# Kernel tuning notes

Measured on AMD Instinct MI355X. Metric: run time of the kernel, lower is better.

## Reference

```python
import jax, jax.numpy as jnp
import numpy as np

T = 100          # sequence length (number of GRU steps)
H = 50           # carry/hidden dim
Z = 10           # latent dim
OUT = Z + Z * (Z + 1) // 2  # 65: mean + tril Cholesky entries
LN_EPS = 1e-6    # flax LayerNorm default epsilon


def setup_inputs() -> dict:
    key = jax.random.key(0)
    ks = jax.random.split(key, 8)
    # Orthogonal-ish recurrent kernels via QR for well-conditioned dynamics
    def ortho(k):
        a = jax.random.normal(k, (H, H), dtype=jnp.float32)
        q, _ = jnp.linalg.qr(a)
        return q
    return {
        "carry_init": jax.random.normal(ks[0], (H,), dtype=jnp.float32),
        "W_hr": ortho(ks[1]), "b_hr": jnp.zeros((H,), jnp.float32),
        "s_r": jnp.ones((H,), jnp.float32), "o_r": jnp.zeros((H,), jnp.float32),
        "W_hz": ortho(ks[2]), "b_hz": jnp.zeros((H,), jnp.float32),
        "s_z": jnp.ones((H,), jnp.float32), "o_z": jnp.zeros((H,), jnp.float32),
        "W_hn": ortho(ks[3]), "b_hn": jnp.zeros((H,), jnp.float32),
        "s_n": jnp.ones((H,), jnp.float32), "o_n": jnp.zeros((H,), jnp.float32),
        "W_dense": jax.random.normal(ks[4], (H, OUT), jnp.float32) * (1.0 / jnp.sqrt(H)),
        "b_dense": jnp.zeros((OUT,), jnp.float32),
    }


def _layernorm(x, scale, bias):
    mu = jnp.mean(x, axis=-1, keepdims=True)
    var = jnp.mean(jnp.square(x - mu), axis=-1, keepdims=True)
    return (x - mu) * jax.lax.rsqrt(var + LN_EPS) * scale + bias


def reference(carry_init, W_hr, b_hr, s_r, o_r, W_hz, b_hz, s_z, o_z,
              W_hn, b_hn, s_n, o_n, W_dense, b_dense):
    # Input to the GRU is zeros((T,1)) -> cell ignores it entirely (no input kernel).
    def step(h, _):
        r = jax.nn.sigmoid(_layernorm(h @ W_hr + b_hr, s_r, o_r))
        z = jax.nn.sigmoid(_layernorm(h @ W_hz + b_hz, s_z, o_z))
        n = jnp.tanh(r * _layernorm(h @ W_hn + b_hn, s_n, o_n))
        new_h = (1.0 - z) * n + z * h
        return new_h, new_h

    _, hs = jax.lax.scan(step, carry_init, None, length=T)  # (T, H)
    out = hs @ W_dense + b_dense                              # (T, OUT)

    tril = jnp.tril_indices(Z)
    eye = jnp.eye(Z, dtype=out.dtype)

    def nat(x):
        mu, flat = x[:Z], x[Z:]
        L = jnp.zeros((Z, Z), dtype=x.dtype).at[tril].set(flat)
        d = jax.nn.softplus(jnp.diagonal(L))  # positive diagonal -> PD Sigma
        L = L.at[jnp.diag_indices(Z)].set(d)
        Sigma = L @ L.T
        # psd_solve: J = Sigma^{-1} via Cholesky solve
        J = jax.scipy.linalg.cho_solve((L, True), eye)
        h_nat = J @ mu
        return Sigma, mu, J, h_nat

    Sigma, mu, J, h_nat = jax.vmap(nat)(out)
    return Sigma, mu, J, h_nat
```

## Files before the change

kernel.cpp:

```cpp
#include <hip/hip_runtime.h>
#include <hip/hip_bf16.h>
#include <math.h>

#define T_STEPS 100
#define H_DIM   50
#define Z_DIM   10
#define OUT_DIM 65

__device__ __forceinline__ float bcast_lane(float v, int lane) {
    return __uint_as_float(__builtin_amdgcn_readlane(__float_as_uint(v), lane));
}

template<int CTRL>
__device__ __forceinline__ float dpp_mov(float x) {
    return __uint_as_float((unsigned)__builtin_amdgcn_update_dpp(
        0, (int)__float_as_uint(x), CTRL, 0xF, 0xF, true));
}

#define DPP_SHR1    0x111
#define DPP_SHR2    0x112
#define DPP_SHR4    0x114
#define DPP_SHR8    0x118
#define DPP_BCAST15 0x142
#define DPP_BCAST31 0x143

__device__ __forceinline__ void wave_sum2(float& a, float& b) {
    a += dpp_mov<DPP_SHR1>(a);    b += dpp_mov<DPP_SHR1>(b);
    a += dpp_mov<DPP_SHR2>(a);    b += dpp_mov<DPP_SHR2>(b);
    a += dpp_mov<DPP_SHR4>(a);    b += dpp_mov<DPP_SHR4>(b);
    a += dpp_mov<DPP_SHR8>(a);    b += dpp_mov<DPP_SHR8>(b);
    a += dpp_mov<DPP_BCAST15>(a); b += dpp_mov<DPP_BCAST15>(b);
    a += dpp_mov<DPP_BCAST31>(a); b += dpp_mov<DPP_BCAST31>(b);
    a = bcast_lane(a, 63);
    b = bcast_lane(b, 63);
}

__device__ __forceinline__ float fast_rcp(float x) { return __builtin_amdgcn_rcpf(x); }
__device__ __forceinline__ float fast_rsq(float x) { return __builtin_amdgcn_rsqf(x); }
__device__ __forceinline__ float fast_sigmoid(float x) {
    return fast_rcp(1.0f + __expf(-x));
}
__device__ __forceinline__ float fast_tanh(float y) {
    return 1.0f - 2.0f * fast_rcp(__expf(2.0f * y) + 1.0f);
}

__global__ __launch_bounds__(256, 1)
void gru_nat_kernel(
    const float* __restrict__ carry_init,
    const float* __restrict__ W_hr, const float* __restrict__ b_hr,
    const float* __restrict__ s_r,  const float* __restrict__ o_r,
    const float* __restrict__ W_hz, const float* __restrict__ b_hz,
    const float* __restrict__ s_z,  const float* __restrict__ o_z,
    const float* __restrict__ W_hn, const float* __restrict__ b_hn,
    const float* __restrict__ s_n,  const float* __restrict__ o_n,
    const float* __restrict__ W_dense, const float* __restrict__ b_dense,
    float* __restrict__ out)
{
    __shared__ float hs[T_STEPS][H_DIM];
    __shared__ float dense[T_STEPS][OUT_DIM];
    __shared__ float share[2][3][64];

    const int tid  = threadIdx.x;
    const int wave = tid >> 6;
    const int lane = tid & 63;

    if (wave < 3) {
        const bool valid = (lane < H_DIM);
        const int  jc    = valid ? lane : 0;

        const float* __restrict__ Wg = (wave == 0) ? W_hr : (wave == 1) ? W_hz : W_hn;
        const float* __restrict__ bg = (wave == 0) ? b_hr : (wave == 1) ? b_hz : b_hn;
        const float* __restrict__ sg = (wave == 0) ? s_r  : (wave == 1) ? s_z  : s_n;
        const float* __restrict__ og = (wave == 0) ? o_r  : (wave == 1) ? o_z  : o_n;

        float w[H_DIM];
        #pragma unroll
        for (int i = 0; i < H_DIM; ++i) w[i] = Wg[i * H_DIM + jc];
        const float bj = bg[jc], sj = sg[jc], oj = og[jc];

        float h = valid ? carry_init[jc] : 0.0f;
        const float invH = 1.0f / (float)H_DIM;

        #pragma unroll 1
        for (int t = 0; t < T_STEPS; ++t) {
            float a0 = bj, a1 = 0.0f, a2 = 0.0f, a3 = 0.0f;
            #pragma unroll
            for (int i = 0; i < 48; i += 4) {
                a0 = fmaf(bcast_lane(h, i + 0), w[i + 0], a0);
                a1 = fmaf(bcast_lane(h, i + 1), w[i + 1], a1);
                a2 = fmaf(bcast_lane(h, i + 2), w[i + 2], a2);
                a3 = fmaf(bcast_lane(h, i + 3), w[i + 3], a3);
            }
            a0 = fmaf(bcast_lane(h, 48), w[48], a0);
            a1 = fmaf(bcast_lane(h, 49), w[49], a1);
            const float a = (a0 + a2) + (a1 + a3);

            float m = valid ? a     : 0.0f;
            float q = valid ? a * a : 0.0f;
            wave_sum2(m, q);

            const float mu   = m * invH;
            const float var  = fmaxf(q * invH - mu * mu, 0.0f);
            const float gval = (a - mu) * fast_rsq(var + 1e-6f) * sj + oj;

            const float sv = (wave == 2) ? gval : fast_sigmoid(gval);
            share[t & 1][wave][lane] = sv;
            __syncthreads();

            const float r  = share[t & 1][0][lane];
            const float z  = share[t & 1][1][lane];
            const float gn = share[t & 1][2][lane];
            const float n  = fast_tanh(r * gn);
            h = n + z * (h - n);
            if (wave == 0 && valid) hs[t][lane] = h;
        }
    } else {
        #pragma unroll 1
        for (int t = 0; t < T_STEPS; ++t) __syncthreads();
    }
    __syncthreads();

    for (int idx = tid; idx < T_STEPS * OUT_DIM; idx += 256) {
        const int t = idx / OUT_DIM;
        const int o = idx - t * OUT_DIM;
        float acc = b_dense[o];
        #pragma unroll 10
        for (int i = 0; i < H_DIM; ++i)
            acc = fmaf(hs[t][i], W_dense[i * OUT_DIM + o], acc);
        dense[t][o] = acc;
    }
    __syncthreads();

    if (tid < T_STEPS) {
        const int t = tid;

        float mu[Z_DIM];
        #pragma unroll
        for (int i = 0; i < Z_DIM; ++i) mu[i] = dense[t][i];

        float L[55];
        #pragma unroll
        for (int f = 0; f < 55; ++f) L[f] = dense[t][Z_DIM + f];

        #pragma unroll
        for (int i = 0; i < Z_DIM; ++i) {
            const int   d = i * (i + 1) / 2 + i;
            const float x = L[d];
            L[d] = (x > 20.0f) ? x : log1pf(__expf(x));
        }

        float* outSigma = out;
        float* outMu    = out + 10000;
        float* outJ     = out + 11000;
        float* outHnat  = out + 21000;

        #pragma unroll
        for (int a = 0; a < Z_DIM; ++a) {
            #pragma unroll
            for (int b = 0; b <= a; ++b) {
                float s = 0.0f;
                #pragma unroll
                for (int k = 0; k <= b; ++k)
                    s = fmaf(L[a * (a + 1) / 2 + k], L[b * (b + 1) / 2 + k], s);
                outSigma[t * 100 + a * 10 + b] = s;
                outSigma[t * 100 + b * 10 + a] = s;
            }
        }

        #pragma unroll
        for (int i = 0; i < Z_DIM; ++i) outMu[t * 10 + i] = mu[i];

        #pragma unroll
        for (int i = 0; i < Z_DIM; ++i) {
            const float d = 1.0f / L[i * (i + 1) / 2 + i];
            float tmp[Z_DIM];
            #pragma unroll
            for (int k = 0; k < Z_DIM - 1; ++k) tmp[k] = 0.0f;
            #pragma unroll
            for (int k = 0; k < i; ++k) {
                float s = 0.0f;
                #pragma unroll
                for (int m = k; m < i; ++m)
                    s = fmaf(L[i * (i + 1) / 2 + m], L[m * (m + 1) / 2 + k], s);
                tmp[k] = -s * d;
            }
            #pragma unroll
            for (int k = 0; k < i; ++k) L[i * (i + 1) / 2 + k] = tmp[k];
            L[i * (i + 1) / 2 + i] = d;
        }

        float hn[Z_DIM];
        #pragma unroll
        for (int a = 0; a < Z_DIM; ++a) hn[a] = 0.0f;

        #pragma unroll
        for (int a = 0; a < Z_DIM; ++a) {
            #pragma unroll
            for (int b = 0; b <= a; ++b) {
                float s = 0.0f;
                #pragma unroll
                for (int m = a; m < Z_DIM; ++m)
                    s = fmaf(L[m * (m + 1) / 2 + a], L[m * (m + 1) / 2 + b], s);
                outJ[t * 100 + a * 10 + b] = s;
                outJ[t * 100 + b * 10 + a] = s;
                hn[a] = fmaf(s, mu[b], hn[a]);
                if (b < a) hn[b] = fmaf(s, mu[a], hn[b]);
            }
        }
        #pragma unroll
        for (int a = 0; a < Z_DIM; ++a) outHnat[t * 10 + a] = hn[a];
    }
}

extern "C" void kernel_launch(void* const* d_in, const int* in_sizes, int n_in,
                              void* d_out, int out_size, void* d_ws, size_t ws_size,
                              hipStream_t stream) {
    const float* p[15];
    for (int i = 0; i < 15; ++i) p[i] = (const float*)d_in[i];
    gru_nat_kernel<<<dim3(1), dim3(256), 0, stream>>>(
        p[0],
        p[1], p[2], p[3], p[4],
        p[5], p[6], p[7], p[8],
        p[9], p[10], p[11], p[12],
        p[13], p[14],
        (float*)d_out);
}
```

Measured before the change: 146.1 us.

## Run all GRU gates in one wave with packed fp16 dot2 matvec

The three-wave GRU recurrence becomes a single 64-lane wave that computes the r, z and n gates together. This removes the per-step block-wide barrier and the shared-memory exchange of gate values. The recurrent weights and the hidden state are packed into fp16 pairs and combined with dot2 instructions, which halves the inner-loop instruction count and the number of readlane broadcasts. The cost is three times the matvec work on one wave, plus reduced precision in the recurrence that could accumulate over 100 steps.

```diff
diff --git a/kernel.cpp b/kernel.cpp
--- a/kernel.cpp
+++ b/kernel.cpp
@@ -6,33 +6,44 @@
 #define H_DIM   50
 #define Z_DIM   10
 #define OUT_DIM 65
+#define KP      25
+
+typedef _Float16 half2v __attribute__((ext_vector_type(2)));
 
 __device__ __forceinline__ float bcast_lane(float v, int lane) {
     return __uint_as_float(__builtin_amdgcn_readlane(__float_as_uint(v), lane));
 }
-
+__device__ __forceinline__ unsigned readlane_u(unsigned v, int lane) {
+    return (unsigned)__builtin_amdgcn_readlane((int)v, lane);
+}
 template<int CTRL>
 __device__ __forceinline__ float dpp_mov(float x) {
     return __uint_as_float((unsigned)__builtin_amdgcn_update_dpp(
         0, (int)__float_as_uint(x), CTRL, 0xF, 0xF, true));
 }
-
-#define DPP_SHR1    0x111
-#define DPP_SHR2    0x112
-#define DPP_SHR4    0x114
-#define DPP_SHR8    0x118
-#define DPP_BCAST15 0x142
-#define DPP_BCAST31 0x143
-
-__device__ __forceinline__ void wave_sum2(float& a, float& b) {
-    a += dpp_mov<DPP_SHR1>(a);    b += dpp_mov<DPP_SHR1>(b);
-    a += dpp_mov<DPP_SHR2>(a);    b += dpp_mov<DPP_SHR2>(b);
-    a += dpp_mov<DPP_SHR4>(a);    b += dpp_mov<DPP_SHR4>(b);
-    a += dpp_mov<DPP_SHR8>(a);    b += dpp_mov<DPP_SHR8>(b);
-    a += dpp_mov<DPP_BCAST15>(a); b += dpp_mov<DPP_BCAST15>(b);
-    a += dpp_mov<DPP_BCAST31>(a); b += dpp_mov<DPP_BCAST31>(b);
-    a = bcast_lane(a, 63);
-    b = bcast_lane(b, 63);
+#define DPP_ROW_SHL1 0x101
+#define DPP_SHR1     0x111
+#define DPP_SHR2     0x112
+#define DPP_SHR4     0x114
+#define DPP_SHR8     0x118
+#define DPP_BCAST15  0x142
+#define DPP_BCAST31  0x143
+
+__device__ __forceinline__ unsigned pack_h2(float lo, float hi) {
+    half2v p;
+    p.x = (_Float16)lo;
+    p.y = (_Float16)hi;
+    return __builtin_bit_cast(unsigned, p);
+}
+__device__ __forceinline__ float fdot2h(unsigned a, unsigned b, float c) {
+#if __has_builtin(__builtin_amdgcn_fdot2)
+    return __builtin_amdgcn_fdot2(__builtin_bit_cast(half2v, a),
+                                  __builtin_bit_cast(half2v, b), c, false);
+#else
+    const half2v x = __builtin_bit_cast(half2v, a);
+    const half2v y = __builtin_bit_cast(half2v, b);
+    return fmaf((float)x.x, (float)y.x, fmaf((float)x.y, (float)y.y, c));
+#endif
 }
 
 __device__ __forceinline__ float fast_rcp(float x) { return __builtin_amdgcn_rcpf(x); }
@@ -58,65 +69,97 @@
 {
     __shared__ float hs[T_STEPS][H_DIM];
     __shared__ float dense[T_STEPS][OUT_DIM];
-    __shared__ float share[2][3][64];
 
     const int tid  = threadIdx.x;
-    const int wave = tid >> 6;
-    const int lane = tid & 63;
-
-    if (wave < 3) {
-        const bool valid = (lane < H_DIM);
-        const int  jc    = valid ? lane : 0;
-
-        const float* __restrict__ Wg = (wave == 0) ? W_hr : (wave == 1) ? W_hz : W_hn;
-        const float* __restrict__ bg = (wave == 0) ? b_hr : (wave == 1) ? b_hz : b_hn;
-        const float* __restrict__ sg = (wave == 0) ? s_r  : (wave == 1) ? s_z  : s_n;
-        const float* __restrict__ og = (wave == 0) ? o_r  : (wave == 1) ? o_z  : o_n;
-
-        float w[H_DIM];
-        #pragma unroll
-        for (int i = 0; i < H_DIM; ++i) w[i] = Wg[i * H_DIM + jc];
-        const float bj = bg[jc], sj = sg[jc], oj = og[jc];
+
+    if (tid < 64) {
+        const int  j     = tid;
+        const bool valid = (j < H_DIM);
+        const int  jc    = valid ? j : 0;
+
+        unsigned wr[KP], wz[KP], wn[KP];
+        #pragma unroll
+        for (int k = 0; k < KP; ++k) {
+            const float r0 = valid ? W_hr[(2 * k)     * H_DIM + jc] : 0.0f;
+            const float r1 = valid ? W_hr[(2 * k + 1) * H_DIM + jc] : 0.0f;
+            const float z0 = valid ? W_hz[(2 * k)     * H_DIM + jc] : 0.0f;
+            const float z1 = valid ? W_hz[(2 * k + 1) * H_DIM + jc] : 0.0f;
+            const float n0 = valid ? W_hn[(2 * k)     * H_DIM + jc] : 0.0f;
+            const float n1 = valid ? W_hn[(2 * k + 1) * H_DIM + jc] : 0.0f;
+            wr[k] = pack_h2(r0, r1);
+            wz[k] = pack_h2(z0, z1);
+            wn[k] = pack_h2(n0, n1);
+        }
+        const float bjr = valid ? b_hr[jc] : 0.0f;
+        const float bjz = valid ? b_hz[jc] : 0.0f;
+        const float bjn = valid ? b_hn[jc] : 0.0f;
+        const float sr  = s_r[jc], og_r = o_r[jc];
+        const float sz  = s_z[jc], og_z = o_z[jc];
+        const float sn  = s_n[jc], og_n = o_n[jc];
 
         float h = valid ? carry_init[jc] : 0.0f;
         const float invH = 1.0f / (float)H_DIM;
 
+        float    hsl = dpp_mov<DPP_ROW_SHL1>(h);
+        unsigned hpk = pack_h2(h, hsl);
+
         #pragma unroll 1
         for (int t = 0; t < T_STEPS; ++t) {
-            float a0 = bj, a1 = 0.0f, a2 = 0.0f, a3 = 0.0f;
-            #pragma unroll
-            for (int i = 0; i < 48; i += 4) {
-                a0 = fmaf(bcast_lane(h, i + 0), w[i + 0], a0);
-                a1 = fmaf(bcast_lane(h, i + 1), w[i + 1], a1);
-                a2 = fmaf(bcast_lane(h, i + 2), w[i + 2], a2);
-                a3 = fmaf(bcast_lane(h, i + 3), w[i + 3], a3);
-            }
-            a0 = fmaf(bcast_lane(h, 48), w[48], a0);
-            a1 = fmaf(bcast_lane(h, 49), w[49], a1);
-            const float a = (a0 + a2) + (a1 + a3);
-
-            float m = valid ? a     : 0.0f;
-            float q = valid ? a * a : 0.0f;
-            wave_sum2(m, q);
-
-            const float mu   = m * invH;
-            const float var  = fmaxf(q * invH - mu * mu, 0.0f);
-            const float gval = (a - mu) * fast_rsq(var + 1e-6f) * sj + oj;
-
-            const float sv = (wave == 2) ? gval : fast_sigmoid(gval);
-            share[t & 1][wave][lane] = sv;
-            __syncthreads();
-
-            const float r  = share[t & 1][0][lane];
-            const float z  = share[t & 1][1][lane];
-            const float gn = share[t & 1][2][lane];
-            const float n  = fast_tanh(r * gn);
+            float ar0 = bjr, ar1 = 0.0f;
+            float az0 = bjz, az1 = 0.0f;
+            float an0 = bjn, an1 = 0.0f;
+            #pragma unroll
+            for (int k = 0; k < KP; k += 2) {
+                const unsigned s0 = readlane_u(hpk, 2 * k);
+                ar0 = fdot2h(s0, wr[k], ar0);
+                az0 = fdot2h(s0, wz[k], az0);
+                an0 = fdot2h(s0, wn[k], an0);
+                if (k + 1 < KP) {
+                    const unsigned s1 = readlane_u(hpk, 2 * (k + 1));
+                    ar1 = fdot2h(s1, wr[k + 1], ar1);
+                    az1 = fdot2h(s1, wz[k + 1], az1);
+                    an1 = fdot2h(s1, wn[k + 1], an1);
+                }
+            }
+            const float ar = ar0 + ar1;
+            const float az = az0 + az1;
+            const float an = an0 + an1;
+
+            float mr = ar, qr = ar * ar;
+            float mz = az, qz = az * az;
+            float mn = an, qn = an * an;
+            #define STAGE(C)                                      \
+                mr += dpp_mov<C>(mr); qr += dpp_mov<C>(qr);       \
+                mz += dpp_mov<C>(mz); qz += dpp_mov<C>(qz);       \
+                mn += dpp_mov<C>(mn); qn += dpp_mov<C>(qn);
+            STAGE(DPP_SHR1) STAGE(DPP_SHR2) STAGE(DPP_SHR4)
+            STAGE(DPP_SHR8) STAGE(DPP_BCAST15) STAGE(DPP_BCAST31)
+            #undef STAGE
+            mr = bcast_lane(mr, 63); qr = bcast_lane(qr, 63);
+            mz = bcast_lane(mz, 63); qz = bcast_lane(qz, 63);
+            mn = bcast_lane(mn, 63); qn = bcast_lane(qn, 63);
+
+            const float mu_r  = mr * invH;
+            const float var_r = fmaxf(qr * invH - mu_r * mu_r, 0.0f);
+            const float g_r   = (ar - mu_r) * fast_rsq(var_r + 1e-6f) * sr + og_r;
+            const float r     = fast_sigmoid(g_r);
+
+            const float mu_z  = mz * invH;
+            const float var_z = fmaxf(qz * invH - mu_z * mu_z, 0.0f);
+            const float g_z   = (az - mu_z) * fast_rsq(var_z + 1e-6f) * sz + og_z;
+            const float z     = fast_sigmoid(g_z);
+
+            const float mu_n  = mn * invH;
+            const float var_n = fmaxf(qn * invH - mu_n * mu_n, 0.0f);
+            const float g_n   = (an - mu_n) * fast_rsq(var_n + 1e-6f) * sn + og_n;
+            const float n     = fast_tanh(r * g_n);
+
             h = n + z * (h - n);
-            if (wave == 0 && valid) hs[t][lane] = h;
-        }
-    } else {
-        #pragma unroll 1
-        for (int t = 0; t < T_STEPS; ++t) __syncthreads();
+            if (valid) hs[t][j] = h;
+
+            hsl = dpp_mov<DPP_ROW_SHL1>(h);
+            hpk = pack_h2(h, hsl);
+        }
     }
     __syncthreads();
 
```

After: 193.0 us. 1.32x slower.
